# Kernel optimization log

Hardware: AMD Instinct MI355X
Metric: run time of the kernel (lower is better)

Reference implementation:

```python
import jax, jax.numpy as jnp
import numpy as np

D = 128  # input_size


def setup_inputs() -> dict:
    key = jax.random.key(0)
    k0, k1, k2, k3 = jax.random.split(key, 4)
    B, S = 4, 4096
    inp = jax.random.normal(k0, (B, S, D), dtype=jnp.float32)
    # nn.Linear weights, stored as [out, in] like torch
    Wq = jax.random.normal(k1, (D, D), dtype=jnp.float32) * (1.0 / np.sqrt(D))
    Wk = jax.random.normal(k2, (D, D), dtype=jnp.float32) * (1.0 / np.sqrt(D))
    Wv = jax.random.normal(k3, (D, D), dtype=jnp.float32) * (1.0 / np.sqrt(D))
    return {"input": inp, "Wq": Wq, "Wk": Wk, "Wv": Wv}


def reference(input, Wq, Wk, Wv):
    # torch Linear: y = x @ W.T
    q = jnp.einsum('bsd,ed->bse', input, Wq)
    k = jnp.einsum('bsd,ed->bse', input, Wk)
    v = jnp.einsum('bsd,ed->bse', input, Wv)
    # NOTE: module divides by input_size (D), not sqrt(D)
    scores = jnp.einsum('bqe,bke->bqk', q, k) / D  # [B,S,S]
    attn = jax.nn.softmax(scores, axis=2)
    return jnp.einsum('bqk,bke->bqe', attn, v)
```

## Files before the change

### kernel.cpp

```cpp
#include <hip/hip_runtime.h>
#include <stdint.h>

#define B_ 4
#define S_ 4096
#define D_ 128
#define KVB 64
#define NT (S_ / KVB)
#define NR (B_ * S_)

typedef __bf16 bf16;
typedef __bf16 bf16x8 __attribute__((ext_vector_type(8)));
typedef float f32x4 __attribute__((ext_vector_type(4)));

#define QB_OFF  0
#define KB_OFF  (QB_OFF + B_*S_*D_*2)
#define VTB_OFF (KB_OFF + B_*S_*D_*2)
#define ACC_OFF (VTB_OFF + B_*S_*D_*2)

#define GLOAD_LDS16(g, l)                                                    \
  __builtin_amdgcn_global_load_lds(                                          \
      (const __attribute__((address_space(1))) void*)(g),                    \
      (__attribute__((address_space(3))) void*)(l), 16, 0, 0)

__global__ __launch_bounds__(256) void proj_kernel(const float* __restrict__ x,
    const float* __restrict__ wq, const float* __restrict__ wk,
    const float* __restrict__ wv, bf16* __restrict__ qb, bf16* __restrict__ kb,
    bf16* __restrict__ vtb) {
  __shared__ bf16 ct[64][136];
  __shared__ __align__(16) bf16 wl[128 * 128];
  const int tid  = threadIdx.x;
  const int wave = tid >> 6, lane = tid & 63;
  const int lrow = lane & 15, g = lane >> 4;
  const int m = blockIdx.y;
  const float* w = (m == 0) ? wq : (m == 1 ? wk : wv);
  const int row0b = blockIdx.x * 64;
  const int row0  = row0b + wave * 16;
  const float SC = 1.4426950408889634f / 128.0f;

#pragma unroll
  for (int it = 0; it < 8; ++it) {
    int chv = it * 256 + tid;
    int row = chv >> 4, pos = chv & 15;
    const float4* wp = (const float4*)(w + (size_t)chv * 8);
    float4 w0 = wp[0], w1 = wp[1];
    bf16x8 v;
    v[0]=(bf16)w0.x; v[1]=(bf16)w0.y; v[2]=(bf16)w0.z; v[3]=(bf16)w0.w;
    v[4]=(bf16)w1.x; v[5]=(bf16)w1.y; v[6]=(bf16)w1.z; v[7]=(bf16)w1.w;
    *(bf16x8*)(&wl[row * 128 + ((pos ^ (row & 15)) * 8)]) = v;
  }

  bf16x8 af[4];
  {
    const float* xp = x + (size_t)(row0 + lrow) * D_ + g * 8;
#pragma unroll
    for (int ks = 0; ks < 4; ++ks) {
      const float4* p4 = (const float4*)(xp + ks * 32);
      float4 a0 = p4[0], a1 = p4[1];
      bf16x8 v;
      v[0]=(bf16)a0.x; v[1]=(bf16)a0.y; v[2]=(bf16)a0.z; v[3]=(bf16)a0.w;
      v[4]=(bf16)a1.x; v[5]=(bf16)a1.y; v[6]=(bf16)a1.z; v[7]=(bf16)a1.w;
      af[ks] = v;
    }
  }
  __syncthreads();

  f32x4 acc[8];
#pragma unroll
  for (int c = 0; c < 8; ++c) acc[c] = (f32x4){0.f, 0.f, 0.f, 0.f};
#pragma unroll
  for (int c = 0; c < 8; ++c) {
#pragma unroll
    for (int ks = 0; ks < 4; ++ks) {
      bf16x8 bf = *(const bf16x8*)(
          &wl[(c * 16 + lrow) * 128 + (((ks * 4 + g) ^ lrow) * 8)]);
      acc[c] = __builtin_amdgcn_mfma_f32_16x16x32_bf16(af[ks], bf, acc[c], 0, 0, 0);
    }
  }
  const float osc = (m == 0) ? SC : 1.0f;
#pragma unroll
  for (int c = 0; c < 8; ++c)
#pragma unroll
    for (int r = 0; r < 4; ++r)
      ct[wave * 16 + g * 4 + r][c * 16 + lrow] = (bf16)(acc[c][r] * osc);
  __syncthreads();

  if (m < 2) {
    bf16* ob = (m == 0) ? qb : kb;
#pragma unroll
    for (int it = 0; it < 4; ++it) {
      int chunk = it * 256 + tid;
      int row = chunk >> 4, pos = chunk & 15;
      *(bf16x8*)(ob + (size_t)(row0b + row) * D_ + pos * 8) =
          *(const bf16x8*)(&ct[row][pos * 8]);
    }
  } else {
    const int b = row0b / S_;
    const int sb = row0b & (S_ - 1);
#pragma unroll
    for (int it = 0; it < 4; ++it) {
      int ci = it * 256 + tid;
      int e = ci >> 3, hc = ci & 7;
      int h = hc >> 2, gg = hc & 3;
      bf16x8 v;
#pragma unroll
      for (int j = 0; j < 8; ++j)
        v[j] = ct[h * 32 + ((j >> 2) * 16 + gg * 4 + (j & 3))][e];
      *(bf16x8*)(vtb + (size_t)(b * D_ + e) * S_ + sb + h * 32 + gg * 8) = v;
    }
  }
}

__global__ __launch_bounds__(256, 2) void attn_kernel(const bf16* __restrict__ qb,
    const bf16* __restrict__ kb, const bf16* __restrict__ vtb,
    float* __restrict__ out, bf16* __restrict__ accP, float* __restrict__ lP,
    int ns) {
  __shared__ __align__(16) bf16 Kt[2][KVB * 128];
  __shared__ __align__(16) bf16 Vt[2][128 * KVB];

  const int tid  = threadIdx.x;
  const int wave = tid >> 6, lane = tid & 63;
  const int lrow = lane & 15, g = lane >> 4;

  const int nwg = gridDim.x;
  int gid = blockIdx.x;
  if ((nwg & 7) == 0) gid = (gid & 7) * (nwg >> 3) + (gid >> 3);
  const int qp  = gid & 127;
  const int seg = gid >> 7;
  const int b   = qp >> 5;
  const int q0  = (qp & 31) * 128 + wave * 32;

  const int base = NT / ns, ext = NT % ns;
  const int cnt  = base + (seg < ext);
  const int t0   = seg * base + (seg < ext ? seg : ext);
  const int tend = t0 + cnt;

  int koff[4], voff[4], kd[4];
#pragma unroll
  for (int it = 0; it < 4; ++it) {
    int ci = (wave * 4 + it) * 64 + lane;
    int krow = ci >> 4, kch = (ci & 15) ^ (krow & 15);
    koff[it] = krow * D_ + kch * 8;
    int d = ci >> 3, vch = (ci & 7) ^ (d & 7);
    voff[it] = d * S_ + vch * 8;
    kd[it] = (wave * 4 + it) * 512;
  }

  bf16x8 qf[2][4];
#pragma unroll
  for (int a = 0; a < 2; ++a) {
    const bf16* qp_ = qb + (size_t)(b * S_ + q0 + a * 16 + lrow) * D_ + g * 8;
#pragma unroll
    for (int ks = 0; ks < 4; ++ks) qf[a][ks] = *(const bf16x8*)(qp_ + ks * 32);
  }

  f32x4 acc[2][8];
#pragma unroll
  for (int a = 0; a < 2; ++a)
#pragma unroll
    for (int c = 0; c < 8; ++c) acc[a][c] = (f32x4){0.f, 0.f, 0.f, 0.f};
  float l_r[2] = {0.f, 0.f};

  const bf16* kbase = kb + (size_t)b * S_ * D_;
  const bf16* vbase = vtb + (size_t)b * D_ * S_;

#define STAGE(tt, buf)                                                       \
  { const bf16* kp_ = kbase + (size_t)(tt) * KVB * D_;                       \
    const bf16* vp_ = vbase + (tt) * KVB;                                    \
    GLOAD_LDS16(kp_ + koff[0], &Kt[buf][kd[0]]);                             \
    GLOAD_LDS16(kp_ + koff[1], &Kt[buf][kd[1]]);                             \
    GLOAD_LDS16(kp_ + koff[2], &Kt[buf][kd[2]]);                             \
    GLOAD_LDS16(kp_ + koff[3], &Kt[buf][kd[3]]);                             \
    GLOAD_LDS16(vp_ + voff[0], &Vt[buf][kd[0]]);                             \
    GLOAD_LDS16(vp_ + voff[1], &Vt[buf][kd[1]]);                             \
    GLOAD_LDS16(vp_ + voff[2], &Vt[buf][kd[2]]);                             \
    GLOAD_LDS16(vp_ + voff[3], &Vt[buf][kd[3]]); }

  STAGE(t0, 0);

  for (int t = t0; t < tend; ++t) {
    const int bcur = (t - t0) & 1;
    asm volatile("s_waitcnt vmcnt(0)\n\ts_barrier" ::: "memory");
    if (t + 1 < tend) STAGE(t + 1, bcur ^ 1);

    f32x4 s[2][4];
#pragma unroll
    for (int a = 0; a < 2; ++a)
#pragma unroll
      for (int ti = 0; ti < 4; ++ti) s[a][ti] = (f32x4){0.f, 0.f, 0.f, 0.f};
    float ts[2] = {0.f, 0.f};
    bf16x8 pa[2][2];
#pragma unroll
    for (int ti = 0; ti < 4; ++ti) {
#pragma unroll
      for (int ks = 0; ks < 4; ++ks) {
        const int row = ti * 16 + lrow;
        bf16x8 kf = *(const bf16x8*)(
            &Kt[bcur][row * 128 + (((ks * 4 + g) ^ lrow) * 8)]);
        s[0][ti] = __builtin_amdgcn_mfma_f32_16x16x32_bf16(kf, qf[0][ks], s[0][ti], 0, 0, 0);
        s[1][ti] = __builtin_amdgcn_mfma_f32_16x16x32_bf16(kf, qf[1][ks], s[1][ti], 0, 0, 0);
      }
      if (ti >= 1) {
        const int j = ti - 1;
#pragma unroll
        for (int a = 0; a < 2; ++a)
#pragma unroll
          for (int r = 0; r < 4; ++r) {
            float e = __builtin_amdgcn_exp2f(s[a][j][r]);
            ts[a] += e;
            pa[a][j >> 1][(j & 1) * 4 + r] = (bf16)e;
          }
      }
    }
#pragma unroll
    for (int a = 0; a < 2; ++a)
#pragma unroll
      for (int r = 0; r < 4; ++r) {
        float e = __builtin_amdgcn_exp2f(s[a][3][r]);
        ts[a] += e;
        pa[a][1][4 + r] = (bf16)e;
      }
    l_r[0] += ts[0];
    l_r[1] += ts[1];

    __builtin_amdgcn_s_setprio(1);
#pragma unroll
    for (int c = 0; c < 8; ++c) {
      const int d = c * 16 + lrow;
#pragma unroll
      for (int bb = 0; bb < 2; ++bb) {
        bf16x8 vf = *(const bf16x8*)(
            &Vt[bcur][d * KVB + (((bb * 4 + g) ^ (d & 7)) * 8)]);
        acc[0][c] = __builtin_amdgcn_mfma_f32_16x16x32_bf16(pa[0][bb], vf, acc[0][c], 0, 0, 0);
        acc[1][c] = __builtin_amdgcn_mfma_f32_16x16x32_bf16(pa[1][bb], vf, acc[1][c], 0, 0, 0);
      }
    }
    __builtin_amdgcn_s_setprio(0);
  }
#undef STAGE

#pragma unroll
  for (int a = 0; a < 2; ++a) {
    l_r[a] += __shfl_xor(l_r[a], 16);
    l_r[a] += __shfl_xor(l_r[a], 32);
  }

  if (ns == 1) {
#pragma unroll
    for (int a = 0; a < 2; ++a) {
      float linv[4];
#pragma unroll
      for (int r = 0; r < 4; ++r) linv[r] = 1.0f / __shfl(l_r[a], g * 4 + r);
#pragma unroll
      for (int c = 0; c < 8; ++c)
#pragma unroll
        for (int r = 0; r < 4; ++r) {
          int row = q0 + a * 16 + g * 4 + r;
          out[(size_t)(b * S_ + row) * D_ + c * 16 + lrow] = acc[a][c][r] * linv[r];
        }
    }
  } else {
#pragma unroll
    for (int a = 0; a < 2; ++a) {
#pragma unroll
      for (int c = 0; c < 8; ++c)
#pragma unroll
        for (int r = 0; r < 4; ++r) {
          int row = b * S_ + q0 + a * 16 + g * 4 + r;
          accP[(((size_t)seg * NR + row) << 7) + c * 16 + lrow] = (bf16)acc[a][c][r];
        }
      if (g == 0) {
        int row = b * S_ + q0 + a * 16 + lrow;
        lP[(size_t)seg * NR + row] = l_r[a];
      }
    }
  }
}

__global__ __launch_bounds__(256) void combine_kernel(const bf16* __restrict__ accP,
    const float* __restrict__ lP, float* __restrict__ out, int ns) {
  const int t = blockIdx.x * 256 + threadIdx.x;
  const int row = t >> 4, d = (t & 15) * 8;
  float L = 0.f;
  float o[8] = {0.f, 0.f, 0.f, 0.f, 0.f, 0.f, 0.f, 0.f};
  for (int i = 0; i < ns; ++i) {
    L += lP[(size_t)i * NR + row];
    bf16x8 a = *(const bf16x8*)(&accP[(((size_t)i * NR + row) << 7) + d]);
#pragma unroll
    for (int j = 0; j < 8; ++j) o[j] += (float)a[j];
  }
  float inv = 1.0f / L;
  float4 o0 = make_float4(o[0]*inv, o[1]*inv, o[2]*inv, o[3]*inv);
  float4 o1 = make_float4(o[4]*inv, o[5]*inv, o[6]*inv, o[7]*inv);
  float* op = &out[(size_t)row * 128 + d];
  *(float4*)op = o0;
  *(float4*)(op + 4) = o1;
}

extern "C" void kernel_launch(void* const* d_in, const int* in_sizes, int n_in,
                              void* d_out, int out_size, void* d_ws, size_t ws_size,
                              hipStream_t stream) {
  const float* x  = (const float*)d_in[0];
  const float* wq = (const float*)d_in[1];
  const float* wk = (const float*)d_in[2];
  const float* wv = (const float*)d_in[3];
  float* out = (float*)d_out;
  char* ws = (char*)d_ws;
  bf16* qb  = (bf16*)(ws + QB_OFF);
  bf16* kb  = (bf16*)(ws + KB_OFF);
  bf16* vtb = (bf16*)(ws + VTB_OFF);

  const size_t acc1 = (size_t)NR * D_ * 2;
  const size_t l1   = (size_t)NR * 4;
  int ns = 4;
  if (ws_size < ACC_OFF + 4 * (acc1 + l1)) ns = 2;
  if (ws_size < ACC_OFF + 2 * (acc1 + l1)) ns = 1;
  bf16* accP = (bf16*)(ws + ACC_OFF);
  float* lp  = (float*)(ws + ACC_OFF + (size_t)ns * acc1);

  hipLaunchKernelGGL(proj_kernel, dim3(256, 3), dim3(256), 0, stream,
                     x, wq, wk, wv, qb, kb, vtb);
  hipLaunchKernelGGL(attn_kernel, dim3(128 * ns), dim3(256), 0, stream,
                     qb, kb, vtb, out, accP, lp, ns);
  if (ns > 1)
    hipLaunchKernelGGL(combine_kernel, dim3(NR / 16), dim3(256), 0, stream,
                       accP, lp, out, ns);
}
```

Baseline: 54.74 us.

## Switch attention to 32x32x16 MFMA tiles with interleaved exp and PV

Rewrites the attention inner loop to use 32x32x16 bf16 MFMA instead of 16x16x32, one 32-row Q tile per wave, with a matching reordered V-transpose layout from the projection kernel and a new LDS swizzle. Exp2 and bf16 packing of the second score tile are interleaved with the PV MFMAs to overlap transcendental work with matrix ops. Larger MFMA tiles cut LDS fragment reads per flop and instruction count, at the cost of larger accumulator register footprint and a layout change that must match between kernels.

```diff
diff --git a/kernel.cpp b/kernel.cpp
--- a/kernel.cpp
+++ b/kernel.cpp
@@ -11,6 +11,7 @@
 typedef __bf16 bf16;
 typedef __bf16 bf16x8 __attribute__((ext_vector_type(8)));
 typedef float f32x4 __attribute__((ext_vector_type(4)));
+typedef float f32x16 __attribute__((ext_vector_type(16)));
 
 #define QB_OFF  0
 #define KB_OFF  (QB_OFF + B_*S_*D_*2)
@@ -99,13 +100,13 @@
 #pragma unroll
     for (int it = 0; it < 4; ++it) {
       int ci = it * 256 + tid;
-      int e = ci >> 3, hc = ci & 7;
-      int h = hc >> 2, gg = hc & 3;
+      int e = ci >> 3, c8 = ci & 7;
+      int h2 = c8 & 1, blk = c8 >> 1;
       bf16x8 v;
 #pragma unroll
       for (int j = 0; j < 8; ++j)
-        v[j] = ct[h * 32 + ((j >> 2) * 16 + gg * 4 + (j & 3))][e];
-      *(bf16x8*)(vtb + (size_t)(b * D_ + e) * S_ + sb + h * 32 + gg * 8) = v;
+        v[j] = ct[blk * 16 + (j >> 2) * 8 + h2 * 4 + (j & 3)][e];
+      *(bf16x8*)(vtb + (size_t)(b * D_ + e) * S_ + sb + c8 * 8) = v;
     }
   }
 }
@@ -115,11 +116,11 @@
     float* __restrict__ out, bf16* __restrict__ accP, float* __restrict__ lP,
     int ns) {
   __shared__ __align__(16) bf16 Kt[2][KVB * 128];
-  __shared__ __align__(16) bf16 Vt[2][128 * KVB];
+  __shared__ __align__(16) bf16 Vt[2][64 * 128];
 
   const int tid  = threadIdx.x;
   const int wave = tid >> 6, lane = tid & 63;
-  const int lrow = lane & 15, g = lane >> 4;
+  const int l31 = lane & 31, h = lane >> 5;
 
   const int nwg = gridDim.x;
   int gid = blockIdx.x;
@@ -140,25 +141,31 @@
     int ci = (wave * 4 + it) * 64 + lane;
     int krow = ci >> 4, kch = (ci & 15) ^ (krow & 15);
     koff[it] = krow * D_ + kch * 8;
-    int d = ci >> 3, vch = (ci & 7) ^ (d & 7);
-    voff[it] = d * S_ + vch * 8;
+    int u = ci >> 4, inner = (ci & 15) ^ (u & 15);
+    int vd = u * 2 + (inner >> 3), vp8 = inner & 7;
+    voff[it] = vd * S_ + vp8 * 8;
     kd[it] = (wave * 4 + it) * 512;
   }
-
-  bf16x8 qf[2][4];
-#pragma unroll
-  for (int a = 0; a < 2; ++a) {
-    const bf16* qp_ = qb + (size_t)(b * S_ + q0 + a * 16 + lrow) * D_ + g * 8;
-#pragma unroll
-    for (int ks = 0; ks < 4; ++ks) qf[a][ks] = *(const bf16x8*)(qp_ + ks * 32);
-  }
-
-  f32x4 acc[2][8];
-#pragma unroll
-  for (int a = 0; a < 2; ++a)
-#pragma unroll
-    for (int c = 0; c < 8; ++c) acc[a][c] = (f32x4){0.f, 0.f, 0.f, 0.f};
-  float l_r[2] = {0.f, 0.f};
+  const int krb0 = l31 * 128;
+  const int krb1 = (32 + l31) * 128;
+  const int kx = l31 & 15;
+  const int vrb = (l31 >> 1) * 128;
+  const int vx = l31 >> 1;
+  const int ib = (lane & 1) * 8;
+
+  bf16x8 qf[8];
+  {
+    const bf16* qp_ = qb + (size_t)(b * S_ + q0 + l31) * D_ + h * 8;
+#pragma unroll
+    for (int ks = 0; ks < 8; ++ks) qf[ks] = *(const bf16x8*)(qp_ + ks * 16);
+  }
+
+  f32x16 acc[4];
+#pragma unroll
+  for (int dt = 0; dt < 4; ++dt)
+#pragma unroll
+    for (int i = 0; i < 16; ++i) acc[dt][i] = 0.f;
+  float l_r = 0.f;
 
   const bf16* kbase = kb + (size_t)b * S_ * D_;
   const bf16* vbase = vtb + (size_t)b * D_ * S_;
@@ -182,96 +189,88 @@
     asm volatile("s_waitcnt vmcnt(0)\n\ts_barrier" ::: "memory");
     if (t + 1 < tend) STAGE(t + 1, bcur ^ 1);
 
-    f32x4 s[2][4];
-#pragma unroll
-    for (int a = 0; a < 2; ++a)
-#pragma unroll
-      for (int ti = 0; ti < 4; ++ti) s[a][ti] = (f32x4){0.f, 0.f, 0.f, 0.f};
-    float ts[2] = {0.f, 0.f};
-    bf16x8 pa[2][2];
-#pragma unroll
-    for (int ti = 0; ti < 4; ++ti) {
-#pragma unroll
-      for (int ks = 0; ks < 4; ++ks) {
-        const int row = ti * 16 + lrow;
-        bf16x8 kf = *(const bf16x8*)(
-            &Kt[bcur][row * 128 + (((ks * 4 + g) ^ lrow) * 8)]);
-        s[0][ti] = __builtin_amdgcn_mfma_f32_16x16x32_bf16(kf, qf[0][ks], s[0][ti], 0, 0, 0);
-        s[1][ti] = __builtin_amdgcn_mfma_f32_16x16x32_bf16(kf, qf[1][ks], s[1][ti], 0, 0, 0);
+    f32x16 s0, s1;
+#pragma unroll
+    for (int i = 0; i < 16; ++i) { s0[i] = 0.f; s1[i] = 0.f; }
+#pragma unroll
+    for (int ks = 0; ks < 8; ++ks) {
+      bf16x8 kf = *(const bf16x8*)(&Kt[bcur][krb0 + (((ks * 2 + h) ^ kx) * 8)]);
+      s0 = __builtin_amdgcn_mfma_f32_32x32x16_bf16(kf, qf[ks], s0, 0, 0, 0);
+    }
+
+    float la = 0.f;
+    bf16x8 pa0, pa1, pa2, pa3;
+#pragma unroll
+    for (int ks = 0; ks < 8; ++ks) {
+      bf16x8 kf = *(const bf16x8*)(&Kt[bcur][krb1 + (((ks * 2 + h) ^ kx) * 8)]);
+      s1 = __builtin_amdgcn_mfma_f32_32x32x16_bf16(kf, qf[ks], s1, 0, 0, 0);
+      float e0 = __builtin_amdgcn_exp2f(s0[ks]);
+      float e1 = __builtin_amdgcn_exp2f(s0[ks + 8]);
+      la += e0 + e1;
+      pa0[ks] = (bf16)e0;
+      pa1[ks] = (bf16)e1;
+    }
+
+    __builtin_amdgcn_s_setprio(1);
+#pragma unroll
+    for (int dt = 0; dt < 4; ++dt) {
+      bf16x8 vf0 = *(const bf16x8*)(
+          &Vt[bcur][dt * 2048 + vrb + (((ib + 0 + h) ^ vx) * 8)]);
+      acc[dt] = __builtin_amdgcn_mfma_f32_32x32x16_bf16(pa0, vf0, acc[dt], 0, 0, 0);
+      float e0 = __builtin_amdgcn_exp2f(s1[2 * dt]);
+      float e1 = __builtin_amdgcn_exp2f(s1[2 * dt + 8]);
+      pa2[2 * dt] = (bf16)e0;
+      pa3[2 * dt] = (bf16)e1;
+      bf16x8 vf1 = *(const bf16x8*)(
+          &Vt[bcur][dt * 2048 + vrb + (((ib + 2 + h) ^ vx) * 8)]);
+      acc[dt] = __builtin_amdgcn_mfma_f32_32x32x16_bf16(pa1, vf1, acc[dt], 0, 0, 0);
+      float e2 = __builtin_amdgcn_exp2f(s1[2 * dt + 1]);
+      float e3 = __builtin_amdgcn_exp2f(s1[2 * dt + 9]);
+      pa2[2 * dt + 1] = (bf16)e2;
+      pa3[2 * dt + 1] = (bf16)e3;
+      la += (e0 + e1) + (e2 + e3);
+    }
+
+#pragma unroll
+    for (int dt = 0; dt < 4; ++dt) {
+      bf16x8 vf2 = *(const bf16x8*)(
+          &Vt[bcur][dt * 2048 + vrb + (((ib + 4 + h) ^ vx) * 8)]);
+      acc[dt] = __builtin_amdgcn_mfma_f32_32x32x16_bf16(pa2, vf2, acc[dt], 0, 0, 0);
+      bf16x8 vf3 = *(const bf16x8*)(
+          &Vt[bcur][dt * 2048 + vrb + (((ib + 6 + h) ^ vx) * 8)]);
+      acc[dt] = __builtin_amdgcn_mfma_f32_32x32x16_bf16(pa3, vf3, acc[dt], 0, 0, 0);
+    }
+    __builtin_amdgcn_s_setprio(0);
+
+    l_r += la;
+  }
+#undef STAGE
+
+  l_r += __shfl_xor(l_r, 32);
+
+  if (ns == 1) {
+    float linv[16];
+#pragma unroll
+    for (int r = 0; r < 16; ++r)
+      linv[r] = 1.0f / __shfl(l_r, (r & 3) + 8 * (r >> 2) + 4 * h);
+#pragma unroll
+    for (int dt = 0; dt < 4; ++dt)
+#pragma unroll
+      for (int r = 0; r < 16; ++r) {
+        int row = q0 + (r & 3) + 8 * (r >> 2) + 4 * h;
+        out[(size_t)(b * S_ + row) * D_ + dt * 32 + l31] = acc[dt][r] * linv[r];
       }
-      if (ti >= 1) {
-        const int j = ti - 1;
-#pragma unroll
-        for (int a = 0; a < 2; ++a)
-#pragma unroll
-          for (int r = 0; r < 4; ++r) {
-            float e = __builtin_amdgcn_exp2f(s[a][j][r]);
-            ts[a] += e;
-            pa[a][j >> 1][(j & 1) * 4 + r] = (bf16)e;
-          }
+  } else {
+#pragma unroll
+    for (int dt = 0; dt < 4; ++dt)
+#pragma unroll
+      for (int r = 0; r < 16; ++r) {
+        int row = b * S_ + q0 + (r & 3) + 8 * (r >> 2) + 4 * h;
+        accP[(((size_t)seg * NR + row) << 7) + dt * 32 + l31] = (bf16)acc[dt][r];
       }
-    }
-#pragma unroll
-    for (int a = 0; a < 2; ++a)
-#pragma unroll
-      for (int r = 0; r < 4; ++r) {
-        float e = __builtin_amdgcn_exp2f(s[a][3][r]);
-        ts[a] += e;
-        pa[a][1][4 + r] = (bf16)e;
-      }
-    l_r[0] += ts[0];
-    l_r[1] += ts[1];
-
-    __builtin_amdgcn_s_setprio(1);
-#pragma unroll
-    for (int c = 0; c < 8; ++c) {
-      const int d = c * 16 + lrow;
-#pragma unroll
-      for (int bb = 0; bb < 2; ++bb) {
-        bf16x8 vf = *(const bf16x8*)(
-            &Vt[bcur][d * KVB + (((bb * 4 + g) ^ (d & 7)) * 8)]);
-        acc[0][c] = __builtin_amdgcn_mfma_f32_16x16x32_bf16(pa[0][bb], vf, acc[0][c], 0, 0, 0);
-        acc[1][c] = __builtin_amdgcn_mfma_f32_16x16x32_bf16(pa[1][bb], vf, acc[1][c], 0, 0, 0);
-      }
-    }
-    __builtin_amdgcn_s_setprio(0);
-  }
-#undef STAGE
-
-#pragma unroll
-  for (int a = 0; a < 2; ++a) {
-    l_r[a] += __shfl_xor(l_r[a], 16);
-    l_r[a] += __shfl_xor(l_r[a], 32);
-  }
-
-  if (ns == 1) {
-#pragma unroll
-    for (int a = 0; a < 2; ++a) {
-      float linv[4];
-#pragma unroll
-      for (int r = 0; r < 4; ++r) linv[r] = 1.0f / __shfl(l_r[a], g * 4 + r);
-#pragma unroll
-      for (int c = 0; c < 8; ++c)
-#pragma unroll
-        for (int r = 0; r < 4; ++r) {
-          int row = q0 + a * 16 + g * 4 + r;
-          out[(size_t)(b * S_ + row) * D_ + c * 16 + lrow] = acc[a][c][r] * linv[r];
-        }
-    }
-  } else {
-#pragma unroll
-    for (int a = 0; a < 2; ++a) {
-#pragma unroll
-      for (int c = 0; c < 8; ++c)
-#pragma unroll
-        for (int r = 0; r < 4; ++r) {
-          int row = b * S_ + q0 + a * 16 + g * 4 + r;
-          accP[(((size_t)seg * NR + row) << 7) + c * 16 + lrow] = (bf16)acc[a][c][r];
-        }
-      if (g == 0) {
-        int row = b * S_ + q0 + a * 16 + lrow;
-        lP[(size_t)seg * NR + row] = l_r[a];
-      }
+    if (lane < 32) {
+      int row = b * S_ + q0 + l31;
+      lP[(size_t)seg * NR + row] = l_r;
     }
   }
 }
```

After: 55.57 us. Within noise of the previous version (+1.5%).
